# Performance work log

Hardware: AMD Instinct MI355X
Metric: run time of the kernel (lower is better)

The kernel has to match this reference:

```python
import jax, jax.numpy as jnp
import numpy as np

NORM = 1.0  # normalization_factor


def _glorot(key, shape):
    fan_in, fan_out = shape
    lim = float(np.sqrt(6.0 / (fan_in + fan_out)))
    return jax.random.uniform(key, shape, jnp.float32, -lim, lim)


def setup_inputs() -> dict:
    key = jax.random.key(0)
    ks = jax.random.split(key, 12)
    B, N = 8, 2048
    latent, hidden, out_dim = 64, 128, 64
    inp = {
        "latent_features": jax.random.normal(ks[0], (B, N, latent), jnp.float32),
        "adjacency_matrix": jax.random.uniform(ks[1], (B, N, N), jnp.float32),
        "node_mask": jnp.ones((B, N, 1), jnp.float32),
        # 3 GCN layers: latent->hidden, hidden->hidden, hidden->hidden
        "W0": _glorot(ks[2], (latent, hidden)), "b0": jnp.zeros((hidden,), jnp.float32),
        "W1": _glorot(ks[3], (hidden, hidden)), "b1": jnp.zeros((hidden,), jnp.float32),
        "W2": _glorot(ks[4], (hidden, hidden)), "b2": jnp.zeros((hidden,), jnp.float32),
        # output projection hidden->out_dim
        "Wout": _glorot(ks[5], (hidden, out_dim)), "bout": jnp.zeros((out_dim,), jnp.float32),
    }
    return inp


def _gcn_layer(h, adj, W, b):
    # message transform (linear), gather+sum aggregate via dense adjacency, ReLU act
    msg = h @ W + b                      # [B,N,dout]
    agg = jnp.einsum('bij,bjd->bid', adj, msg) / NORM  # sum aggregation over neighbors
    return jax.nn.relu(agg)


def reference(latent_features, adjacency_matrix, node_mask,
              W0, b0, W1, b1, W2, b2, Wout, bout):
    h = _gcn_layer(latent_features, adjacency_matrix, W0, b0)
    h = _gcn_layer(h, adjacency_matrix, W1, b1)
    h = _gcn_layer(h, adjacency_matrix, W2, b2)
    # output projection + node mask
    return (h @ Wout + bout) * node_mask
```

## Files before the change

### kernel.cpp

```cpp
#include <hip/hip_runtime.h>
#include <hip/hip_bf16.h>


typedef __bf16 bf16;
typedef __bf16 bf16x4 __attribute__((ext_vector_type(4)));
typedef __bf16 bf16x8 __attribute__((ext_vector_type(8)));
typedef float  f32x16 __attribute__((ext_vector_type(16)));
typedef float  f32x4  __attribute__((ext_vector_type(4)));

static __device__ inline f32x16 mfma32(bf16x8 a, bf16x8 b, f32x16 c) {
    return __builtin_amdgcn_mfma_f32_32x32x16_bf16(a, b, c, 0, 0, 0);
}

static __device__ inline void tile_barrier() {
    asm volatile("s_waitcnt lgkmcnt(0)" ::: "memory");
    __builtin_amdgcn_s_barrier();
    asm volatile("" ::: "memory");
}

static __device__ inline void glds16(const bf16* g, bf16* l) {
    __builtin_amdgcn_global_load_lds(
        (const __attribute__((address_space(1))) unsigned int*)g,
        (__attribute__((address_space(3))) unsigned int*)l, 16, 0, 0);
}

#define NB   8
#define NN   2048
#define LAT  64
#define HID  128
#define ODIM 64
#define BM   64
#define BK   128
#define NP   16
#define LDK  136
#define HLD  136

__global__ __launch_bounds__(256) void prep_t0_k(
    const float* __restrict__ lat, const float* __restrict__ W0,
    const float* __restrict__ b0,
    const float* __restrict__ W1, const float* __restrict__ W2,
    const float* __restrict__ Wout,
    bf16* __restrict__ msgT, bf16* __restrict__ WT1,
    bf16* __restrict__ WT2, bf16* __restrict__ WoutT)
{
    __shared__ __align__(16) bf16 WTs[HID * 72];
    int tid = threadIdx.x;
    int blk = blockIdx.x;

    if (blk >= 256) {
        int i = (blk - 256) * 256 + tid;
        if (i < HID * HID) { int fo = i >> 7, k = i & 127; WT1[i] = (bf16)W1[k * HID + fo]; return; }
        i -= HID * HID;
        if (i < HID * HID) { int fo = i >> 7, k = i & 127; WT2[i] = (bf16)W2[k * HID + fo]; return; }
        i -= HID * HID;
        if (i < ODIM * HID) { int o = i >> 7, k = i & 127; WoutT[i] = (bf16)Wout[k * ODIM + o]; return; }
        return;
    }

    for (int i = tid; i < LAT * HID; i += 256) {
        int k = i >> 7, fo = i & 127;
        WTs[fo * 72 + k] = (bf16)W0[i];
    }
    __syncthreads();

    int l = tid & 63, w = tid >> 6;
    int lm = l & 31, lh = l >> 5;
    int g0 = blk * 64;
    int b  = g0 >> 11, nb = g0 & 2047;

    const bf16*  Wrow = &WTs[(w * 32 + lm) * 72 + lh * 8];
    const float* r0   = lat + (size_t)(g0 + lm) * LAT + lh * 8;
    const float* r1   = r0 + (size_t)32 * LAT;

    f32x16 acc0 = {}, acc1 = {};
#pragma unroll
    for (int k0 = 0; k0 < LAT; k0 += 16) {
        bf16x8 a = *(const bf16x8*)(Wrow + k0);
        f32x4 x0 = *(const f32x4*)(r0 + k0), x1 = *(const f32x4*)(r0 + k0 + 4);
        f32x4 y0 = *(const f32x4*)(r1 + k0), y1 = *(const f32x4*)(r1 + k0 + 4);
        bf16x8 v0, v1;
        v0[0]=(bf16)x0[0]; v0[1]=(bf16)x0[1]; v0[2]=(bf16)x0[2]; v0[3]=(bf16)x0[3];
        v0[4]=(bf16)x1[0]; v0[5]=(bf16)x1[1]; v0[6]=(bf16)x1[2]; v0[7]=(bf16)x1[3];
        v1[0]=(bf16)y0[0]; v1[1]=(bf16)y0[1]; v1[2]=(bf16)y0[2]; v1[3]=(bf16)y0[3];
        v1[4]=(bf16)y1[0]; v1[5]=(bf16)y1[1]; v1[6]=(bf16)y1[2]; v1[7]=(bf16)y1[3];
        acc0 = mfma32(a, v0, acc0);
        acc1 = mfma32(a, v1, acc1);
    }

    bf16* outb = msgT + (size_t)b * (HID * NN) + nb;
#pragma unroll
    for (int r = 0; r < 16; ++r) {
        int fo = w * 32 + (r & 3) + 8 * (r >> 2) + 4 * lh;
        float bv = b0[fo];
        outb[(size_t)fo * NN + lm]      = (bf16)(acc0[r] + bv);
        outb[(size_t)fo * NN + 32 + lm] = (bf16)(acc1[r] + bv);
    }
}

__global__ __launch_bounds__(512) void agg_f32_k(
    const float* __restrict__ adjf, bf16* __restrict__ adjbo,
    const bf16* __restrict__ msgT, const bf16* __restrict__ WTn,
    const float* __restrict__ biasn, bf16* __restrict__ msg_out)
{
    __shared__ __align__(16) bf16 As[2][BM * LDK];
    __shared__ __align__(16) bf16 Bs[2][HID * LDK];
    __shared__ __align__(16) bf16 Hs[BM * HLD];
    int tid = threadIdx.x;
    int l = tid & 63, w = tid >> 6;
    int lm = l & 31, lh = l >> 5;
    int wm = w >> 2, wn = w & 3;
    int b  = blockIdx.x & 7;
    int m0 = (blockIdx.x >> 3) * BM;

    const bf16* msgb = msgT + (size_t)b * (HID * NN);
    int br = tid >> 3, bc8 = (tid & 7) * 8;
    const bf16* bsrc = msgb + (size_t)br * NN + bc8;

    int ar = tid >> 3, acf = (tid & 7) * 4;
    const float* asrc = adjf  + (size_t)b * NN * NN + (size_t)(m0 + ar) * NN + acf;
    bf16*        adst = adjbo + (size_t)b * NN * NN + (size_t)(m0 + ar) * NN + acf;

    f32x4  fa[2][4];
    bf16x8 pb[2][4];

    auto loadTile = [&](int set, int k) {
#pragma unroll
        for (int g = 0; g < 4; ++g) fa[set][g] = *(const f32x4*)(asrc + k + g * 32);
#pragma unroll
        for (int h = 0; h < 2; ++h)
#pragma unroll
            for (int g = 0; g < 2; ++g)
                pb[set][h * 2 + g] = *(const bf16x8*)(bsrc + (size_t)(h * 64) * NN + k + g * 64);
    };
    auto storeTile = [&](int set, int buf, int k) {
#pragma unroll
        for (int g = 0; g < 4; ++g) {
            bf16x4 v;
            v[0]=(bf16)fa[set][g][0]; v[1]=(bf16)fa[set][g][1];
            v[2]=(bf16)fa[set][g][2]; v[3]=(bf16)fa[set][g][3];
            *(bf16x4*)&As[buf][ar * LDK + acf + g * 32] = v;
            *(bf16x4*)(adst + k + g * 32)               = v;
        }
#pragma unroll
        for (int h = 0; h < 2; ++h)
#pragma unroll
            for (int g = 0; g < 2; ++g)
                *(bf16x8*)&Bs[buf][(br + h * 64) * LDK + bc8 + g * 64] = pb[set][h * 2 + g];
    };

    f32x16 acc = {};
    auto mfmaTile = [&](int buf) {
        const bf16* Ac = &As[buf][(wm * 32 + lm) * LDK + lh * 8];
        const bf16* Bc = &Bs[buf][(wn * 32 + lm) * LDK + lh * 8];
#pragma unroll
        for (int s = 0; s < 8; ++s)
            acc = mfma32(*(const bf16x8*)(Ac + s * 16), *(const bf16x8*)(Bc + s * 16), acc);
    };

    loadTile(0, 0 * BK);
    loadTile(1, 1 * BK);
    storeTile(0, 0, 0 * BK);
    tile_barrier();

#define PHASE(U)                                                               \
    do {                                                                       \
        int q = qb + (U);                                                      \
        if (q + 2 < NP) loadTile((U), (q + 2) * BK);                           \
        if (q + 1 < NP) storeTile(((U) + 1) & 1, ((U) + 1) & 1, (q + 1) * BK); \
        mfmaTile((U) & 1);                                                     \
        tile_barrier();                                                        \
    } while (0)

#pragma unroll 1
    for (int qb = 0; qb < NP; qb += 2) {
        PHASE(0);
        PHASE(1);
    }
#undef PHASE

#pragma unroll
    for (int r = 0; r < 16; ++r) {
        int row = wm * 32 + (r & 3) + 8 * (r >> 2) + 4 * lh;
        float v = acc[r];
        Hs[row * HLD + wn * 32 + lm] = (bf16)(v > 0.f ? v : 0.f);
    }
    __syncthreads();

    const bf16* Arow = WTn + (size_t)(wn * 32 + lm) * HID + lh * 8;
    const bf16* Brow = &Hs[(wm * 32 + lm) * HLD + lh * 8];
    f32x16 acc2 = {};
#pragma unroll
    for (int s = 0; s < 8; ++s)
        acc2 = mfma32(*(const bf16x8*)(Arow + s * 16), *(const bf16x8*)(Brow + s * 16), acc2);
    bf16* outb = msg_out + (size_t)b * (HID * NN) + m0 + wm * 32;
#pragma unroll
    for (int r = 0; r < 16; ++r) {
        int fo = wn * 32 + (r & 3) + 8 * (r >> 2) + 4 * lh;
        outb[(size_t)fo * NN + lm] = (bf16)(acc2[r] + biasn[fo]);
    }
}

template<int MODE>
__global__ __launch_bounds__(512) void aggg_k(
    const bf16* __restrict__ adjb,
    const bf16* __restrict__ msgT, const bf16* __restrict__ WTn,
    const float* __restrict__ biasn, bf16* __restrict__ msg_out,
    const float* __restrict__ mask, float* __restrict__ out)
{
    __shared__ __align__(16) bf16 As[2][BM * BK];
    __shared__ __align__(16) bf16 Bs[2][HID * BK];
    __shared__ __align__(16) bf16 Hs[BM * HLD];
    int tid = threadIdx.x;
    int l = tid & 63, wv = tid >> 6;
    int lm = l & 31, lh = l >> 5;
    int wm = wv >> 2, wn = wv & 3;
    int b  = blockIdx.x & 7;
    int m0 = (blockIdx.x >> 3) * BM;

    int r4 = l >> 4, c16 = l & 15;

    const bf16* adjbase = adjb + (size_t)b * NN * NN + (size_t)m0 * NN;
    const bf16* msgb    = msgT + (size_t)b * (HID * NN);

    int ar0 = wv * 8 + r4, ar1 = ar0 + 4;
    const bf16* aS0 = adjbase + (size_t)ar0 * NN + ((c16 ^ (ar0 & 7)) * 8);
    const bf16* aS1 = adjbase + (size_t)ar1 * NN + ((c16 ^ (ar1 & 7)) * 8);
    int br0 = wv * 16 + r4;
    const bf16* bS0 = msgb + (size_t)(br0     ) * NN + ((c16 ^ ((br0     ) & 7)) * 8);
    const bf16* bS1 = msgb + (size_t)(br0 +  4) * NN + ((c16 ^ ((br0 +  4) & 7)) * 8);
    const bf16* bS2 = msgb + (size_t)(br0 +  8) * NN + ((c16 ^ ((br0 +  8) & 7)) * 8);
    const bf16* bS3 = msgb + (size_t)(br0 + 12) * NN + ((c16 ^ ((br0 + 12) & 7)) * 8);

    auto stage = [&](int buf, int k) {
        glds16(aS0 + k, &As[buf][(wv * 8     ) * BK]);
        glds16(aS1 + k, &As[buf][(wv * 8 +  4) * BK]);
        glds16(bS0 + k, &Bs[buf][(wv * 16    ) * BK]);
        glds16(bS1 + k, &Bs[buf][(wv * 16 + 4) * BK]);
        glds16(bS2 + k, &Bs[buf][(wv * 16 + 8) * BK]);
        glds16(bS3 + k, &Bs[buf][(wv * 16 +12) * BK]);
    };

    f32x16 acc = {};
    auto mfmaTile = [&](int buf) {
        int arow = wm * 32 + lm;
        int brow = wn * 32 + lm;
        const bf16* Abase = &As[buf][arow * BK];
        const bf16* Bbase = &Bs[buf][brow * BK];
        int h = lm & 7;
#pragma unroll
        for (int s = 0; s < 8; ++s) {
            int ca = ((lh + 2 * s) ^ h) * 8;
            acc = mfma32(*(const bf16x8*)(Abase + ca), *(const bf16x8*)(Bbase + ca), acc);
        }
    };

    stage(0, 0);
    stage(1, BK);

#pragma unroll 1
    for (int t = 0; t < NP; ++t) {
        if (t < NP - 1) asm volatile("s_waitcnt vmcnt(6)" ::: "memory");
        else            asm volatile("s_waitcnt vmcnt(0)" ::: "memory");
        __builtin_amdgcn_s_barrier();
        mfmaTile(t & 1);
        asm volatile("" ::: "memory");
        __builtin_amdgcn_s_barrier();
        if (t + 2 < NP) stage(t & 1, (t + 2) * BK);
    }

#pragma unroll
    for (int r = 0; r < 16; ++r) {
        int row = wm * 32 + (r & 3) + 8 * (r >> 2) + 4 * lh;
        float v = acc[r];
        Hs[row * HLD + wn * 32 + lm] = (bf16)(v > 0.f ? v : 0.f);
    }
    __syncthreads();

    if (MODE == 0) {
        const bf16* Arow = WTn + (size_t)(wn * 32 + lm) * HID + lh * 8;
        const bf16* Brow = &Hs[(wm * 32 + lm) * HLD + lh * 8];
        f32x16 acc2 = {};
#pragma unroll
        for (int s = 0; s < 8; ++s)
            acc2 = mfma32(*(const bf16x8*)(Arow + s * 16), *(const bf16x8*)(Brow + s * 16), acc2);
        bf16* outb = msg_out + (size_t)b * (HID * NN) + m0 + wm * 32;
#pragma unroll
        for (int r = 0; r < 16; ++r) {
            int fo = wn * 32 + (r & 3) + 8 * (r >> 2) + 4 * lh;
            outb[(size_t)fo * NN + lm] = (bf16)(acc2[r] + biasn[fo]);
        }
    } else {
        if (wn < 2) {
            int ob = wn * 32;
            const bf16* Arow = &Hs[(wm * 32 + lm) * HLD + lh * 8];
            const bf16* Brow = WTn + (size_t)(ob + lm) * HID + lh * 8;
            f32x16 acc2 = {};
#pragma unroll
            for (int s = 0; s < 8; ++s)
                acc2 = mfma32(*(const bf16x8*)(Arow + s * 16), *(const bf16x8*)(Brow + s * 16), acc2);
            float bv = biasn[ob + lm];
#pragma unroll
            for (int r = 0; r < 16; ++r) {
                int node = wm * 32 + (r & 3) + 8 * (r >> 2) + 4 * lh;
                int g = b * NN + m0 + node;
                out[(size_t)g * ODIM + ob + lm] = (acc2[r] + bv) * mask[g];
            }
        }
    }
}

extern "C" void kernel_launch(void* const* d_in, const int* in_sizes, int n_in,
                              void* d_out, int out_size, void* d_ws, size_t ws_size,
                              hipStream_t stream)
{
    const float* lat  = (const float*)d_in[0];
    const float* adj  = (const float*)d_in[1];
    const float* mask = (const float*)d_in[2];
    const float* W0   = (const float*)d_in[3];
    const float* b0   = (const float*)d_in[4];
    const float* W1   = (const float*)d_in[5];
    const float* b1   = (const float*)d_in[6];
    const float* W2   = (const float*)d_in[7];
    const float* b2   = (const float*)d_in[8];
    const float* Wout = (const float*)d_in[9];
    const float* bout = (const float*)d_in[10];
    float* out = (float*)d_out;

    char* ws = (char*)d_ws;
    bf16* msgA  = (bf16*)(ws + 0);
    bf16* msgB  = (bf16*)(ws + 4194304);
    bf16* adjbf = (bf16*)(ws + 8388608);
    bf16* WT1   = (bf16*)(ws + 75497472);
    bf16* WT2   = (bf16*)(ws + 75530240);
    bf16* WoutT = (bf16*)(ws + 75563008);

    prep_t0_k<<<416, 256, 0, stream>>>(lat, W0, b0, W1, W2, Wout, msgA, WT1, WT2, WoutT);

    agg_f32_k<<<256, 512, 0, stream>>>(adj, adjbf, msgA, WT1, b1, msgB);
    aggg_k<0><<<256, 512, 0, stream>>>(adjbf, msgB, WT2, b2, msgA, nullptr, nullptr);
    aggg_k<1><<<256, 512, 0, stream>>>(adjbf, msgA, WoutT, bout, nullptr, mask, out);
}
```

Baseline: 278.7 us.

## Interleave next-tile loads with MFMA phases and widen LDS swizzle to 16

Replaces the two-tile-ahead prefetch with a one-tile-ahead scheme. The next tile's global-to-LDS loads are split into three chunks issued between four MFMA phases, each phase ending in a barrier. The XOR swizzle now uses 16 rows instead of 8 to cut LDS bank conflicts, and s_setprio raises wave priority around the MFMAs. The loop now waits on vmcnt(0) every iteration and adds a barrier per phase, so global load latency may be less hidden and sync overhead goes up.

```diff
diff --git a/kernel.cpp b/kernel.cpp
--- a/kernel.cpp
+++ b/kernel.cpp
@@ -201,7 +201,7 @@
 }
 
 template<int MODE>
-__global__ __launch_bounds__(512) void aggg_k(
+__global__ __launch_bounds__(512) void agg8_k(
     const bf16* __restrict__ adjb,
     const bf16* __restrict__ msgT, const bf16* __restrict__ WTn,
     const float* __restrict__ biasn, bf16* __restrict__ msg_out,
@@ -223,49 +223,60 @@
     const bf16* msgb    = msgT + (size_t)b * (HID * NN);
 
     int ar0 = wv * 8 + r4, ar1 = ar0 + 4;
-    const bf16* aS0 = adjbase + (size_t)ar0 * NN + ((c16 ^ (ar0 & 7)) * 8);
-    const bf16* aS1 = adjbase + (size_t)ar1 * NN + ((c16 ^ (ar1 & 7)) * 8);
+    const bf16* aS0 = adjbase + (size_t)ar0 * NN + ((c16 ^ (ar0 & 15)) * 8);
+    const bf16* aS1 = adjbase + (size_t)ar1 * NN + ((c16 ^ (ar1 & 15)) * 8);
     int br0 = wv * 16 + r4;
-    const bf16* bS0 = msgb + (size_t)(br0     ) * NN + ((c16 ^ ((br0     ) & 7)) * 8);
-    const bf16* bS1 = msgb + (size_t)(br0 +  4) * NN + ((c16 ^ ((br0 +  4) & 7)) * 8);
-    const bf16* bS2 = msgb + (size_t)(br0 +  8) * NN + ((c16 ^ ((br0 +  8) & 7)) * 8);
-    const bf16* bS3 = msgb + (size_t)(br0 + 12) * NN + ((c16 ^ ((br0 + 12) & 7)) * 8);
-
-    auto stage = [&](int buf, int k) {
+    const bf16* bS0 = msgb + (size_t)(br0     ) * NN + ((c16 ^ ((br0     ) & 15)) * 8);
+    const bf16* bS1 = msgb + (size_t)(br0 +  4) * NN + ((c16 ^ ((br0 +  4) & 15)) * 8);
+    const bf16* bS2 = msgb + (size_t)(br0 +  8) * NN + ((c16 ^ ((br0 +  8) & 15)) * 8);
+    const bf16* bS3 = msgb + (size_t)(br0 + 12) * NN + ((c16 ^ ((br0 + 12) & 15)) * 8);
+
+    auto sA  = [&](int buf, int k) {
         glds16(aS0 + k, &As[buf][(wv * 8     ) * BK]);
         glds16(aS1 + k, &As[buf][(wv * 8 +  4) * BK]);
+    };
+    auto sB0 = [&](int buf, int k) {
         glds16(bS0 + k, &Bs[buf][(wv * 16    ) * BK]);
         glds16(bS1 + k, &Bs[buf][(wv * 16 + 4) * BK]);
+    };
+    auto sB1 = [&](int buf, int k) {
         glds16(bS2 + k, &Bs[buf][(wv * 16 + 8) * BK]);
         glds16(bS3 + k, &Bs[buf][(wv * 16 +12) * BK]);
     };
 
+    int arow = wm * 32 + lm, brow = wn * 32 + lm;
+    int hA = arow & 15, hB = brow & 15;
     f32x16 acc = {};
-    auto mfmaTile = [&](int buf) {
-        int arow = wm * 32 + lm;
-        int brow = wn * 32 + lm;
-        const bf16* Abase = &As[buf][arow * BK];
-        const bf16* Bbase = &Bs[buf][brow * BK];
-        int h = lm & 7;
-#pragma unroll
-        for (int s = 0; s < 8; ++s) {
-            int ca = ((lh + 2 * s) ^ h) * 8;
-            acc = mfma32(*(const bf16x8*)(Abase + ca), *(const bf16x8*)(Bbase + ca), acc);
-        }
-    };
-
-    stage(0, 0);
-    stage(1, BK);
+
+    sA(0, 0); sB0(0, 0); sB1(0, 0);
 
 #pragma unroll 1
     for (int t = 0; t < NP; ++t) {
-        if (t < NP - 1) asm volatile("s_waitcnt vmcnt(6)" ::: "memory");
-        else            asm volatile("s_waitcnt vmcnt(0)" ::: "memory");
+        int buf = t & 1, nbuf = buf ^ 1;
+        int kn = (t + 1) * BK;
+        asm volatile("s_waitcnt vmcnt(0)" ::: "memory");
         __builtin_amdgcn_s_barrier();
-        mfmaTile(t & 1);
-        asm volatile("" ::: "memory");
-        __builtin_amdgcn_s_barrier();
-        if (t + 2 < NP) stage(t & 1, (t + 2) * BK);
+        const bf16* Ab = &As[buf][arow * BK];
+        const bf16* Bb = &Bs[buf][brow * BK];
+#pragma unroll
+        for (int p = 0; p < 4; ++p) {
+            if (t + 1 < NP) {
+                if      (p == 0) sA (nbuf, kn);
+                else if (p == 1) sB0(nbuf, kn);
+                else if (p == 2) sB1(nbuf, kn);
+            }
+            bf16x8 a0 = *(const bf16x8*)(Ab + ((4 * p     + lh) ^ hA) * 8);
+            bf16x8 b0 = *(const bf16x8*)(Bb + ((4 * p     + lh) ^ hB) * 8);
+            bf16x8 a1 = *(const bf16x8*)(Ab + ((4 * p + 2 + lh) ^ hA) * 8);
+            bf16x8 b1 = *(const bf16x8*)(Bb + ((4 * p + 2 + lh) ^ hB) * 8);
+            asm volatile("s_waitcnt lgkmcnt(0)" ::: "memory");
+            __builtin_amdgcn_sched_barrier(0);
+            __builtin_amdgcn_s_setprio(1);
+            acc = mfma32(a0, b0, acc);
+            acc = mfma32(a1, b1, acc);
+            __builtin_amdgcn_s_setprio(0);
+            __builtin_amdgcn_s_barrier();
+        }
     }
 
 #pragma unroll
@@ -337,6 +348,6 @@
     prep_t0_k<<<416, 256, 0, stream>>>(lat, W0, b0, W1, W2, Wout, msgA, WT1, WT2, WoutT);
 
     agg_f32_k<<<256, 512, 0, stream>>>(adj, adjbf, msgA, WT1, b1, msgB);
-    aggg_k<0><<<256, 512, 0, stream>>>(adjbf, msgB, WT2, b2, msgA, nullptr, nullptr);
-    aggg_k<1><<<256, 512, 0, stream>>>(adjbf, msgA, WoutT, bout, nullptr, mask, out);
-}
+    agg8_k<0><<<256, 512, 0, stream>>>(adjbf, msgB, WT2, b2, msgA, nullptr, nullptr);
+    agg8_k<1><<<256, 512, 0, stream>>>(adjbf, msgA, WoutT, bout, nullptr, mask, out);
+}
```

Result: slower. 297.2 us (+6.6%).
